# Performance work log

Measured on AMD Instinct MI355X. Metric: run time of the kernel, lower is better.

Reference implementation:

```python
import jax, jax.numpy as jnp
import numpy as np
from jax.scipy.special import logsumexp

HIDDEN = 512
KEY_DIM = HIDDEN // 8  # 64
B, N, M = 4, 2048, 2048
EPS_IN = 1e-5  # InstanceNorm2d default eps
N_ITERS = 20


def setup_inputs() -> dict:
    key = jax.random.key(0)
    k = jax.random.split(key, 6)
    bound = 1.0 / np.sqrt(HIDDEN)  # nn.Linear default init range
    return {
        "x": jax.random.normal(k[0], (B, N, HIDDEN), dtype=jnp.float32),
        "y": jax.random.normal(k[1], (B, M, HIDDEN), dtype=jnp.float32),
        "Wq": jax.random.uniform(k[2], (KEY_DIM, HIDDEN), jnp.float32, -bound, bound),
        "bq": jax.random.uniform(k[3], (KEY_DIM,), jnp.float32, -bound, bound),
        "in_w": jnp.ones((1,), jnp.float32),   # InstanceNorm2d affine weight
        "in_b": jnp.zeros((1,), jnp.float32),  # InstanceNorm2d affine bias
    }


def _sinkhorn_slack(log_alpha, n_iters):
    # log_alpha: [B, J, K]; pad with a zero slack row and column -> [B, J+1, K+1]
    la = jnp.pad(log_alpha, ((0, 0), (0, 1), (0, 1)))

    def step(la, _):
        top = la[:, :-1, :]
        top = top - logsumexp(top, axis=2, keepdims=True)
        la = jnp.concatenate([top, la[:, -1:, :]], axis=1)
        left = la[:, :, :-1]
        left = left - logsumexp(left, axis=1, keepdims=True)
        la = jnp.concatenate([left, la[:, :, -1:]], axis=2)
        return la, None

    la, _ = jax.lax.scan(step, la, None, length=n_iters)
    return la[:, :-1, :-1]


def reference(x, y, Wq, bq, in_w, in_b):
    # linear projection to key_dim
    xw = jnp.einsum('bnh,kh->bnk', x, Wq) + bq  # [B,N,K]
    yw = jnp.einsum('bmh,kh->bmk', y, Wq) + bq  # [B,M,K]
    # pairwise squared euclidean distance [B,N,M]
    dist = (jnp.sum(xw * xw, axis=-1)[:, :, None]
            + jnp.sum(yw * yw, axis=-1)[:, None, :]
            - 2.0 * jnp.einsum('bnk,bmk->bnm', xw, yw))
    e = jnp.exp(-dist)
    # InstanceNorm2d(1, affine=True): normalize each [N,M] map per batch element
    mean = jnp.mean(e, axis=(1, 2), keepdims=True)
    var = jnp.mean((e - mean) ** 2, axis=(1, 2), keepdims=True)
    dist_s = (e - mean) / jnp.sqrt(var + EPS_IN) * in_w[0] + in_b[0]
    # 20-iter slack Sinkhorn in log space
    log_ds = _sinkhorn_slack(dist_s, N_ITERS)
    ds = jnp.exp(log_ds)
    atweight = jnp.max(ds, axis=-1, keepdims=True)  # [B,N,1]
    attention = jnp.einsum('bni,bmi->bnm', atweight, atweight)  # [B,N,N]
    return attention
```

## Files before the change

kernel.cpp:

```cpp
#include <hip/hip_runtime.h>
#include <hip/hip_bf16.h>

constexpr int B = 4, N = 2048, M = 2048, H = 512, ITERS = 20;
constexpr float EPS_IN = 1e-5f;
constexpr float LOG2E = 1.4426950408889634f;
constexpr float LN2 = 0.6931471805599453f;

typedef unsigned short ushort_t;
typedef unsigned int uint_t;
typedef __attribute__((ext_vector_type(8))) short bf16x8;
typedef __attribute__((ext_vector_type(4))) float f32x4;

__device__ __forceinline__ float fexp2(float x) { return __builtin_amdgcn_exp2f(x); }
__device__ __forceinline__ float flog2(float x) { return __builtin_amdgcn_logf(x); }
__device__ __forceinline__ float blo(uint_t v) { return __uint_as_float(v << 16); }
__device__ __forceinline__ float bhi(uint_t v) { return __uint_as_float(v & 0xffff0000u); }
__device__ __forceinline__ uint_t bf16rn(float f) {
  uint_t x = __float_as_uint(f);
  return (x + 0x7fffu + ((x >> 16) & 1u)) >> 16;
}

__global__ __launch_bounds__(256) void wqconv_kernel(
    const float* __restrict__ Wq, ushort_t* __restrict__ wqh) {
  int g = blockIdx.x * 256 + threadIdx.x;
  float4 v = *(const float4*)(Wq + (size_t)g * 4);
  uint2 pk;
  pk.x = bf16rn(v.x) | (bf16rn(v.y) << 16);
  pk.y = bf16rn(v.z) | (bf16rn(v.w) << 16);
  *(uint2*)(wqh + (size_t)g * 4) = pk;
}

__global__ __launch_bounds__(256) void proj_kernel(
    const float* __restrict__ x, const float* __restrict__ y,
    const ushort_t* __restrict__ wqh, const float* __restrict__ bq,
    ushort_t* __restrict__ qwh, float* __restrict__ norms,
    float* __restrict__ stats) {
  int t = threadIdx.x;
  if (blockIdx.x == 0 && t < 32) stats[t] = 0.0f;
  int w = t >> 6, lane = t & 63;
  int fr = lane & 15, fh = (lane >> 4) * 8;
  int rw = blockIdx.x * 64 + w * 16;
  int row = rw + fr;
  const float* src = (row < B * N) ? x + (size_t)row * H
                                   : y + (size_t)(row - B * N) * H;

  f32x4 acc[4];
#pragma unroll
  for (int j = 0; j < 4; j++) acc[j] = (f32x4){0.f, 0.f, 0.f, 0.f};

#pragma unroll
  for (int ks = 0; ks < 16; ks++) {
    float4 a0 = *(const float4*)(src + ks * 32 + fh);
    float4 a1 = *(const float4*)(src + ks * 32 + fh + 4);
    union { uint4 u; bf16x8 h; } ac;
    ac.u.x = bf16rn(a0.x) | (bf16rn(a0.y) << 16);
    ac.u.y = bf16rn(a0.z) | (bf16rn(a0.w) << 16);
    ac.u.z = bf16rn(a1.x) | (bf16rn(a1.y) << 16);
    ac.u.w = bf16rn(a1.z) | (bf16rn(a1.w) << 16);
    bf16x8 aF = ac.h;
#pragma unroll
    for (int j = 0; j < 4; j++) {
      bf16x8 bF = *(const bf16x8*)(wqh + (size_t)(j * 16 + fr) * H + ks * 32 + fh);
      acc[j] = __builtin_amdgcn_mfma_f32_16x16x32_bf16(aF, bF, acc[j], 0, 0, 0);
    }
  }

  float bqv[4];
#pragma unroll
  for (int j = 0; j < 4; j++) bqv[j] = bq[j * 16 + fr];

#pragma unroll
  for (int reg = 0; reg < 4; reg++) {
    int r = rw + ((lane >> 4) << 2) + reg;
    float nr = 0.0f;
#pragma unroll
    for (int j = 0; j < 4; j++) {
      float vv = acc[j][reg] + bqv[j];
      qwh[(size_t)r * 64 + j * 16 + fr] = (ushort_t)bf16rn(vv);
      nr = fmaf(vv, vv, nr);
    }
    nr += __shfl_xor(nr, 1, 64);
    nr += __shfl_xor(nr, 2, 64);
    nr += __shfl_xor(nr, 4, 64);
    nr += __shfl_xor(nr, 8, 64);
    if (fr == 0) norms[r] = nr;
  }
}

__global__ __launch_bounds__(256) void dist_kernel(
    const ushort_t* __restrict__ qwh, const float* __restrict__ norms,
    ushort_t* __restrict__ e, float* __restrict__ stats) {
  __shared__ __align__(16) ushort_t eT[128 * 136];
  __shared__ float xnL[128], ynL[128], scr[12];
  int t = threadIdx.x;
  int b = blockIdx.z;
  int n0 = blockIdx.x * 128, m0 = blockIdx.y * 128;
  int w = t >> 6, lane = t & 63;

  if (t < 128) xnL[t] = norms[b * N + n0 + t];
  else ynL[t - 128] = norms[B * N + b * M + m0 + (t - 128)];

  int wr = (w >> 1) * 64, wc = (w & 1) * 64;
  int fr = lane & 15, fk = (lane >> 4) * 8;

  f32x4 acc[4][4];
#pragma unroll
  for (int i = 0; i < 4; i++)
#pragma unroll
    for (int j = 0; j < 4; j++) acc[i][j] = (f32x4){0.f, 0.f, 0.f, 0.f};

  const ushort_t* xb = qwh + (size_t)(b * N + n0 + wr + fr) * 64 + fk;
  const ushort_t* yb = qwh + (size_t)(B * N + b * M + m0 + wc + fr) * 64 + fk;
#pragma unroll
  for (int kg = 0; kg < 2; kg++) {
    bf16x8 aF[4], bF[4];
#pragma unroll
    for (int i = 0; i < 4; i++) {
      aF[i] = *(const bf16x8*)(xb + (size_t)i * 16 * 64 + kg * 32);
      bF[i] = *(const bf16x8*)(yb + (size_t)i * 16 * 64 + kg * 32);
    }
#pragma unroll
    for (int i = 0; i < 4; i++)
#pragma unroll
      for (int j = 0; j < 4; j++)
        acc[i][j] = __builtin_amdgcn_mfma_f32_16x16x32_bf16(
            aF[i], bF[j], acc[i][j], 0, 0, 0);
  }
  __syncthreads();

  float lsum = 0.0f, lsq = 0.0f, lmax = 0.0f;
#pragma unroll
  for (int i = 0; i < 4; i++) {
    int rl = wr + i * 16 + ((lane >> 4) << 2);
    float xn0 = xnL[rl], xn1 = xnL[rl + 1], xn2 = xnL[rl + 2], xn3 = xnL[rl + 3];
#pragma unroll
    for (int j = 0; j < 4; j++) {
      int cl = wc + j * 16 + (lane & 15);
      float yn_ = ynL[cl];
      float v0 = __expf(-(xn0 + yn_ - 2.0f * acc[i][j][0]));
      float v1 = __expf(-(xn1 + yn_ - 2.0f * acc[i][j][1]));
      float v2 = __expf(-(xn2 + yn_ - 2.0f * acc[i][j][2]));
      float v3 = __expf(-(xn3 + yn_ - 2.0f * acc[i][j][3]));
      lsum += (v0 + v1) + (v2 + v3);
      lsq += (v0 * v0 + v1 * v1) + (v2 * v2 + v3 * v3);
      lmax = fmaxf(fmaxf(lmax, fmaxf(v0, v1)), fmaxf(v2, v3));
      eT[(rl + 0) * 136 + cl] = (ushort_t)bf16rn(v0);
      eT[(rl + 1) * 136 + cl] = (ushort_t)bf16rn(v1);
      eT[(rl + 2) * 136 + cl] = (ushort_t)bf16rn(v2);
      eT[(rl + 3) * 136 + cl] = (ushort_t)bf16rn(v3);
    }
  }
#pragma unroll
  for (int off = 32; off; off >>= 1) {
    lsum += __shfl_xor(lsum, off, 64);
    lsq += __shfl_xor(lsq, off, 64);
    lmax = fmaxf(lmax, __shfl_xor(lmax, off, 64));
  }
  if (lane == 0) { scr[w] = lsum; scr[4 + w] = lsq; scr[8 + w] = lmax; }
  __syncthreads();

#pragma unroll
  for (int p = 0; p < 8; p++) {
    int row = p * 16 + (t >> 4);
    int cs = (t & 15) * 8;
    uint4 vv = *(const uint4*)&eT[row * 136 + cs];
    *(uint4*)(e + (size_t)(b * N + n0 + row) * M + m0 + cs) = vv;
  }
  if (t == 0) {
    float ssum = scr[0] + scr[1] + scr[2] + scr[3];
    float ssq = scr[4] + scr[5] + scr[6] + scr[7];
    float smax = fmaxf(fmaxf(scr[8], scr[9]), fmaxf(scr[10], scr[11]));
    atomicAdd(&stats[b * 4 + 0], ssum);
    atomicAdd(&stats[b * 4 + 1], ssq);
    atomicMax((unsigned int*)&stats[b * 4 + 2], __float_as_uint(smax));
  }
}

__global__ void params_csinit_kernel(const float* __restrict__ stats,
                                     const float* __restrict__ in_w,
                                     const float* __restrict__ in_b,
                                     float* __restrict__ params,
                                     float* __restrict__ csb) {
  int g = blockIdx.x * 256 + threadIdx.x;
  *(float4*)(csb + g * 4) = float4{0.f, 0.f, 0.f, 0.f};
  if (blockIdx.x == 0 && threadIdx.x < B) {
    int b = threadIdx.x;
    float NMf = (float)N * (float)M;
    float mean = stats[b * 4 + 0] / NMf;
    float var = stats[b * 4 + 1] / NMf - mean * mean;
    var = fmaxf(var, 0.0f);
    float stdv = sqrtf(var + EPS_IN);
    float s = in_w[0] / stdv;
    float t = in_b[0] - mean * s;
    float emax = __uint_as_float(((const unsigned int*)stats)[b * 4 + 2]);
    float Amax = fmaxf(fmaf(s, emax, t), t);
    float KK = fmaxf(Amax - 60.0f, 0.0f);
    params[b * 8 + 0] = s * LOG2E;
    params[b * 8 + 1] = (t - 2.0f * KK) * LOG2E;
    params[b * 8 + 2] = KK;
    params[b * 8 + 3] = __expf(-KK);
    params[b * 8 + 4] = __expf(KK);
  }
}

#define PASS1(uu, off, PA, PB)                           \
  {                                                      \
    float4 ca = *(const float4*)&C2a[(off) + ln4];       \
    float4 cb = *(const float4*)&C2b[(off) + ln4];       \
    PA.x = fexp2(fmaf(blo(uu.x), sL, ca.x));             \
    PA.y = fexp2(fmaf(bhi(uu.x), sL, ca.y));             \
    PA.z = fexp2(fmaf(blo(uu.y), sL, ca.z));             \
    PA.w = fexp2(fmaf(bhi(uu.y), sL, ca.w));             \
    PB.x = fexp2(fmaf(blo(uu.z), sL, cb.x));             \
    PB.y = fexp2(fmaf(bhi(uu.z), sL, cb.y));             \
    PB.z = fexp2(fmaf(blo(uu.w), sL, cb.z));             \
    PB.w = fexp2(fmaf(bhi(uu.w), sL, cb.w));             \
    s0 += PA.x + PB.x;                                   \
    s1 += PA.y + PB.y;                                   \
    s2 += PA.z + PB.z;                                   \
    s3 += PA.w + PB.w;                                   \
  }

#define PASS2(PA, PB, AA, BB)                            \
  {                                                      \
    AA.x = fmaf(PA.x, g, AA.x);                          \
    AA.y = fmaf(PA.y, g, AA.y);                          \
    AA.z = fmaf(PA.z, g, AA.z);                          \
    AA.w = fmaf(PA.w, g, AA.w);                          \
    BB.x = fmaf(PB.x, g, BB.x);                          \
    BB.y = fmaf(PB.y, g, BB.y);                          \
    BB.z = fmaf(PB.z, g, BB.z);                          \
    BB.w = fmaf(PB.w, g, BB.w);                          \
  }

#define DO_ROW(q0, q1, q2, q3, ridx)                                   \
  {                                                                    \
    float s0 = 0, s1 = 0, s2 = 0, s3 = 0;                              \
    PASS1(q0, 0, pA0, pB0)                                             \
    PASS1(q1, 256, pA1, pB1)                                           \
    PASS1(q2, 512, pA2, pB2)                                           \
    PASS1(q3, 768, pA3, pB3)                                           \
    float sum = (s0 + s1) + (s2 + s3);                                 \
    _Pragma("unroll")                                                  \
    for (int off = 32; off; off >>= 1) sum += __shfl_xor(sum, off, 64);\
    float sumtot = sum + enk;                                          \
    float ls = flog2(sumtot);                                          \
    if (lane == 0) R[b * N + (ridx)] = KK + LN2 * ls;                  \
    float g = fexp2(-KK * LOG2E - ls);                                 \
    PASS2(pA0, pB0, accA0, accB0)                                      \
    PASS2(pA1, pB1, accA1, accB1)                                      \
    PASS2(pA2, pB2, accA2, accB2)                                      \
    PASS2(pA3, pB3, accA3, accB3)                                      \
  }

__global__ __launch_bounds__(256) void sink_pass(
    const ushort_t* __restrict__ e, const float* __restrict__ params,
    const float* __restrict__ cs_cur, float* __restrict__ cs_nxt,
    float* __restrict__ cs_zz, float* __restrict__ R) {
  __shared__ __align__(16) float C2a[1024], C2b[1024];
  __shared__ __align__(16) float Ds[2048];
  __shared__ __align__(16) float colA[1024], colB[1024];
  int t = threadIdx.x;
  int b = blockIdx.y, blk = blockIdx.x;
  int w = t >> 6, lane = t & 63;
  int ln4 = lane * 4;
  const float* pr = params + b * 8;
  float sL = pr[0], c0L = pr[1], KK = pr[2], enk = pr[3], ekk = pr[4];

  int r0 = blk * 16 + w * 4;
  const ushort_t* ep = e + (size_t)(b * N + r0) * M + lane * 8;
  uint4 u0 = *(const uint4*)(ep);
  uint4 u1 = *(const uint4*)(ep + 512);
  uint4 u2 = *(const uint4*)(ep + 1024);
  uint4 u3 = *(const uint4*)(ep + 1536);
  const ushort_t* ep2 = ep + M;
  uint4 v0 = *(const uint4*)(ep2);
  uint4 v1 = *(const uint4*)(ep2 + 512);
  uint4 v2 = *(const uint4*)(ep2 + 1024);
  uint4 v3 = *(const uint4*)(ep2 + 1536);

  if (blk == 0) {
#pragma unroll
    for (int k = 0; k < 2; k++)
      *(float4*)(cs_zz + b * M + (k * 256 + t) * 4) = float4{0.f, 0.f, 0.f, 0.f};
  }
  {
    float4 c0 = *(const float4*)(cs_cur + b * M + t * 8);
    float4 c1 = *(const float4*)(cs_cur + b * M + t * 8 + 4);
    c0.x += enk; c0.y += enk; c0.z += enk; c0.w += enk;
    c1.x += enk; c1.y += enk; c1.z += enk; c1.w += enk;
    float4 ca, cb;
    ca.x = c0L - flog2(c0.x); ca.y = c0L - flog2(c0.y);
    ca.z = c0L - flog2(c0.z); ca.w = c0L - flog2(c0.w);
    cb.x = c0L - flog2(c1.x); cb.y = c0L - flog2(c1.y);
    cb.z = c0L - flog2(c1.z); cb.w = c0L - flog2(c1.w);
    *(float4*)&C2a[w * 256 + ln4] = ca;
    *(float4*)&C2b[w * 256 + ln4] = cb;
    float4 d0 = {ekk * c0.x, ekk * c0.y, ekk * c0.z, ekk * c0.w};
    float4 d1 = {ekk * c1.x, ekk * c1.y, ekk * c1.z, ekk * c1.w};
    *(float4*)&Ds[t * 8] = d0;
    *(float4*)&Ds[t * 8 + 4] = d1;
  }
  __syncthreads();

  float4 accA0 = {0,0,0,0}, accA1 = {0,0,0,0}, accA2 = {0,0,0,0}, accA3 = {0,0,0,0};
  float4 accB0 = {0,0,0,0}, accB1 = {0,0,0,0}, accB2 = {0,0,0,0}, accB3 = {0,0,0,0};
  float4 pA0, pA1, pA2, pA3, pB0, pB1, pB2, pB3;

  DO_ROW(u0, u1, u2, u3, r0)
  {
    const ushort_t* ep3 = ep + 2 * M;
    u0 = *(const uint4*)(ep3);
    u1 = *(const uint4*)(ep3 + 512);
    u2 = *(const uint4*)(ep3 + 1024);
    u3 = *(const uint4*)(ep3 + 1536);
  }
  DO_ROW(v0, v1, v2, v3, r0 + 1)
  {
    const ushort_t* ep4 = ep + 3 * M;
    v0 = *(const uint4*)(ep4);
    v1 = *(const uint4*)(ep4 + 512);
    v2 = *(const uint4*)(ep4 + 1024);
    v3 = *(const uint4*)(ep4 + 1536);
  }
  DO_ROW(u0, u1, u2, u3, r0 + 2)
  DO_ROW(v0, v1, v2, v3, r0 + 3)

  for (int ww = 0; ww < 4; ww++) {
    if (w == ww) {
      if (ww == 0) {
        *(float4*)&colA[ln4] = accA0;
        *(float4*)&colA[256 + ln4] = accA1;
        *(float4*)&colA[512 + ln4] = accA2;
        *(float4*)&colA[768 + ln4] = accA3;
        *(float4*)&colB[ln4] = accB0;
        *(float4*)&colB[256 + ln4] = accB1;
        *(float4*)&colB[512 + ln4] = accB2;
        *(float4*)&colB[768 + ln4] = accB3;
      } else {
        float4 q;
        q = *(float4*)&colA[ln4];
        q.x += accA0.x; q.y += accA0.y; q.z += accA0.z; q.w += accA0.w;
        *(float4*)&colA[ln4] = q;
        q = *(float4*)&colA[256 + ln4];
        q.x += accA1.x; q.y += accA1.y; q.z += accA1.z; q.w += accA1.w;
        *(float4*)&colA[256 + ln4] = q;
        q = *(float4*)&colA[512 + ln4];
        q.x += accA2.x; q.y += accA2.y; q.z += accA2.z; q.w += accA2.w;
        *(float4*)&colA[512 + ln4] = q;
        q = *(float4*)&colA[768 + ln4];
        q.x += accA3.x; q.y += accA3.y; q.z += accA3.z; q.w += accA3.w;
        *(float4*)&colA[768 + ln4] = q;
        q = *(float4*)&colB[ln4];
        q.x += accB0.x; q.y += accB0.y; q.z += accB0.z; q.w += accB0.w;
        *(float4*)&colB[ln4] = q;
        q = *(float4*)&colB[256 + ln4];
        q.x += accB1.x; q.y += accB1.y; q.z += accB1.z; q.w += accB1.w;
        *(float4*)&colB[256 + ln4] = q;
        q = *(float4*)&colB[512 + ln4];
        q.x += accB2.x; q.y += accB2.y; q.z += accB2.z; q.w += accB2.w;
        *(float4*)&colB[512 + ln4] = q;
        q = *(float4*)&colB[768 + ln4];
        q.x += accB3.x; q.y += accB3.y; q.z += accB3.z; q.w += accB3.w;
        *(float4*)&colB[768 + ln4] = q;
      }
    }
    __syncthreads();
  }
  {
    int q = t & 7;
    const float* srcb = (q < 4) ? colA : colB;
    int qq = q & 3;
#pragma unroll
    for (int k = 0; k < 8; k++) {
      int j = k * 256 + t;
      int idx = (j >> 9) * 256 + ((j >> 3) & 63) * 4 + qq;
      atomicAdd(&cs_nxt[b * M + j], srcb[idx] * Ds[j]);
    }
  }
}

__global__ __launch_bounds__(256) void awmax_kernel(
    const ushort_t* __restrict__ e, const float* __restrict__ params,
    const float* __restrict__ cs_fin, const float* __restrict__ R,
    float* __restrict__ aw) {
  __shared__ __align__(16) float C2a[1024], C2b[1024];
  int t = threadIdx.x;
  int b = blockIdx.y, blk = blockIdx.x;
  const float* pr = params + b * 8;
  float sL = pr[0], c0L = pr[1], KK = pr[2], enk = pr[3];
  {
    float4 v0 = *(const float4*)(cs_fin + b * M + t * 8);
    float4 v1 = *(const float4*)(cs_fin + b * M + t * 8 + 4);
    float4 ca, cb;
    ca.x = c0L - flog2(v0.x + enk); ca.y = c0L - flog2(v0.y + enk);
    ca.z = c0L - flog2(v0.z + enk); ca.w = c0L - flog2(v0.w + enk);
    cb.x = c0L - flog2(v1.x + enk); cb.y = c0L - flog2(v1.y + enk);
    cb.z = c0L - flog2(v1.z + enk); cb.w = c0L - flog2(v1.w + enk);
    int it = t >> 6, ln = t & 63;
    *(float4*)&C2a[it * 256 + ln * 4] = ca;
    *(float4*)&C2b[it * 256 + ln * 4] = cb;
  }
  __syncthreads();

  int w = t >> 6, lane = t & 63;
  int ln4 = lane * 4;
  int r0 = blk * 16 + w * 4;
  const ushort_t* erow = e + (size_t)(b * N + r0) * M;
#pragma unroll
  for (int rr = 0; rr < 4; rr++) {
    float mx = -3.4e38f;
#pragma unroll
    for (int it = 0; it < 4; it++) {
      uint4 u = *(const uint4*)(erow + (size_t)rr * M + it * 512 + lane * 8);
      float4 ca = *(const float4*)&C2a[it * 256 + ln4];
      float4 cb = *(const float4*)&C2b[it * 256 + ln4];
      mx = fmaxf(mx, fmaf(blo(u.x), sL, ca.x));
      mx = fmaxf(mx, fmaf(bhi(u.x), sL, ca.y));
      mx = fmaxf(mx, fmaf(blo(u.y), sL, ca.z));
      mx = fmaxf(mx, fmaf(bhi(u.y), sL, ca.w));
      mx = fmaxf(mx, fmaf(blo(u.z), sL, cb.x));
      mx = fmaxf(mx, fmaf(bhi(u.z), sL, cb.y));
      mx = fmaxf(mx, fmaf(blo(u.w), sL, cb.z));
      mx = fmaxf(mx, fmaf(bhi(u.w), sL, cb.w));
    }
#pragma unroll
    for (int off = 32; off; off >>= 1) mx = fmaxf(mx, __shfl_xor(mx, off, 64));
    if (lane == 0) {
      float Rr = R[b * N + r0 + rr];
      aw[b * N + r0 + rr] = fexp2(mx + (KK - Rr) * LOG2E);
    }
  }
}

__global__ __launch_bounds__(256) void outer_kernel(const float* __restrict__ aw,
                                                    float* __restrict__ out) {
  size_t idx = (size_t)blockIdx.x * 256 + threadIdx.x;
  int b = (int)(idx >> 20);
  size_t rem = idx & ((1u << 20) - 1);
  int n = (int)(rem >> 9);
  int m4 = (int)(rem & 511) << 2;
  float a = aw[b * N + n];
  float4 wv = *(const float4*)(aw + b * N + m4);
  float4 o = {a * wv.x, a * wv.y, a * wv.z, a * wv.w};
  *(float4*)(out + (idx << 2)) = o;
}

extern "C" void kernel_launch(void* const* d_in, const int* in_sizes, int n_in,
                              void* d_out, int out_size, void* d_ws, size_t ws_size,
                              hipStream_t stream) {
  const float* x = (const float*)d_in[0];
  const float* y = (const float*)d_in[1];
  const float* Wq = (const float*)d_in[2];
  const float* bq = (const float*)d_in[3];
  const float* in_w = (const float*)d_in[4];
  const float* in_b = (const float*)d_in[5];
  ushort_t* e = (ushort_t*)d_out;

  float* ws = (float*)d_ws;
  ushort_t* qwh = (ushort_t*)ws;
  float* norms = ws + 1048576;
  float* R = norms + 16384;
  float* csb0 = R + 8192;
  float* csb1 = csb0 + 8192;
  float* csb2 = csb1 + 8192;
  float* aw = csb2 + 8192;
  float* stats = aw + 8192;
  float* params = stats + 32;
  ushort_t* wqh = (ushort_t*)(params + 32);
  float* csb[3] = {csb0, csb1, csb2};

  wqconv_kernel<<<32, 256, 0, stream>>>(Wq, wqh);
  proj_kernel<<<256, 256, 0, stream>>>(x, y, wqh, bq, qwh, norms, stats);
  dist_kernel<<<dim3(16, 16, B), 256, 0, stream>>>(qwh, norms, e, stats);
  params_csinit_kernel<<<24, 256, 0, stream>>>(stats, in_w, in_b, params, csb0);

  for (int it = 0; it < ITERS; it++) {
    sink_pass<<<dim3(128, B), 256, 0, stream>>>(
        e, params, csb[it % 3], csb[(it + 1) % 3], csb[(it + 2) % 3], R);
  }
  awmax_kernel<<<dim3(128, B), 256, 0, stream>>>(e, params, csb[ITERS % 3], R, aw);
  outer_kernel<<<16384, 256, 0, stream>>>(aw, (float*)d_out);
}
```

Measured before the change: 307.3 us.

## Double sinkhorn block size to 512 threads and pre-swizzle projection layout for MFMA

The Sinkhorn pass now uses 512-thread blocks that each cover 32 rows, with half as many blocks. Column partials go into two shared-memory accumulators that are summed before the atomic adds, which halves the number of global atomics per column. Separately, the projection output is written in a fragment-contiguous layout so the distance kernel's MFMA operand loads become fully coalesced per lane. The cost is fewer blocks in the Sinkhorn pass (256 total), which may lower parallelism, plus more shared memory per block.

```diff
diff --git a/kernel.cpp b/kernel.cpp
--- a/kernel.cpp
+++ b/kernel.cpp
@@ -33,7 +33,7 @@
 __global__ __launch_bounds__(256) void proj_kernel(
     const float* __restrict__ x, const float* __restrict__ y,
     const ushort_t* __restrict__ wqh, const float* __restrict__ bq,
-    ushort_t* __restrict__ qwh, float* __restrict__ norms,
+    ushort_t* __restrict__ qwf, float* __restrict__ norms,
     float* __restrict__ stats) {
   int t = threadIdx.x;
   if (blockIdx.x == 0 && t < 32) stats[t] = 0.0f;
@@ -69,14 +69,17 @@
 #pragma unroll
   for (int j = 0; j < 4; j++) bqv[j] = bq[j * 16 + fr];
 
+  size_t gbase = (size_t)(rw >> 4) * 1024;
 #pragma unroll
   for (int reg = 0; reg < 4; reg++) {
-    int r = rw + ((lane >> 4) << 2) + reg;
+    int rr = ((lane >> 4) << 2) + reg;
+    int r = rw + rr;
     float nr = 0.0f;
 #pragma unroll
     for (int j = 0; j < 4; j++) {
       float vv = acc[j][reg] + bqv[j];
-      qwh[(size_t)r * 64 + j * 16 + fr] = (ushort_t)bf16rn(vv);
+      qwf[gbase + (size_t)(j * 2 + (fr >> 3)) * 128 + rr * 8 + (fr & 7)] =
+          (ushort_t)bf16rn(vv);
       nr = fmaf(vv, vv, nr);
     }
     nr += __shfl_xor(nr, 1, 64);
@@ -88,7 +91,7 @@
 }
 
 __global__ __launch_bounds__(256) void dist_kernel(
-    const ushort_t* __restrict__ qwh, const float* __restrict__ norms,
+    const ushort_t* __restrict__ qwf, const float* __restrict__ norms,
     ushort_t* __restrict__ e, float* __restrict__ stats) {
   __shared__ __align__(16) ushort_t eT[128 * 136];
   __shared__ float xnL[128], ynL[128], scr[12];
@@ -101,7 +104,6 @@
   else ynL[t - 128] = norms[B * N + b * M + m0 + (t - 128)];
 
   int wr = (w >> 1) * 64, wc = (w & 1) * 64;
-  int fr = lane & 15, fk = (lane >> 4) * 8;
 
   f32x4 acc[4][4];
 #pragma unroll
@@ -109,15 +111,15 @@
 #pragma unroll
     for (int j = 0; j < 4; j++) acc[i][j] = (f32x4){0.f, 0.f, 0.f, 0.f};
 
-  const ushort_t* xb = qwh + (size_t)(b * N + n0 + wr + fr) * 64 + fk;
-  const ushort_t* yb = qwh + (size_t)(B * N + b * M + m0 + wc + fr) * 64 + fk;
+  const ushort_t* xg = qwf + (size_t)((b * N + n0 + wr) >> 4) * 1024 + lane * 8;
+  const ushort_t* yg = qwf + (size_t)((B * N + b * M + m0 + wc) >> 4) * 1024 + lane * 8;
 #pragma unroll
   for (int kg = 0; kg < 2; kg++) {
     bf16x8 aF[4], bF[4];
 #pragma unroll
     for (int i = 0; i < 4; i++) {
-      aF[i] = *(const bf16x8*)(xb + (size_t)i * 16 * 64 + kg * 32);
-      bF[i] = *(const bf16x8*)(yb + (size_t)i * 16 * 64 + kg * 32);
+      aF[i] = *(const bf16x8*)(xg + (size_t)i * 1024 + kg * 512);
+      bF[i] = *(const bf16x8*)(yg + (size_t)i * 1024 + kg * 512);
     }
 #pragma unroll
     for (int i = 0; i < 4; i++)
@@ -253,13 +255,55 @@
     PASS2(pA3, pB3, accA3, accB3)                                      \
   }
 
-__global__ __launch_bounds__(256) void sink_pass(
+#define COMBINE8(cA, cB)                                               \
+  {                                                                    \
+    float4 q;                                                          \
+    q = *(float4*)&cA[ln4];                                            \
+    q.x += accA0.x; q.y += accA0.y; q.z += accA0.z; q.w += accA0.w;    \
+    *(float4*)&cA[ln4] = q;                                            \
+    q = *(float4*)&cA[256 + ln4];                                      \
+    q.x += accA1.x; q.y += accA1.y; q.z += accA1.z; q.w += accA1.w;    \
+    *(float4*)&cA[256 + ln4] = q;                                      \
+    q = *(float4*)&cA[512 + ln4];                                      \
+    q.x += accA2.x; q.y += accA2.y; q.z += accA2.z; q.w += accA2.w;    \
+    *(float4*)&cA[512 + ln4] = q;                                      \
+    q = *(float4*)&cA[768 + ln4];                                      \
+    q.x += accA3.x; q.y += accA3.y; q.z += accA3.z; q.w += accA3.w;    \
+    *(float4*)&cA[768 + ln4] = q;                                      \
+    q = *(float4*)&cB[ln4];                                            \
+    q.x += accB0.x; q.y += accB0.y; q.z += accB0.z; q.w += accB0.w;    \
+    *(float4*)&cB[ln4] = q;                                            \
+    q = *(float4*)&cB[256 + ln4];                                      \
+    q.x += accB1.x; q.y += accB1.y; q.z += accB1.z; q.w += accB1.w;    \
+    *(float4*)&cB[256 + ln4] = q;                                      \
+    q = *(float4*)&cB[512 + ln4];                                      \
+    q.x += accB2.x; q.y += accB2.y; q.z += accB2.z; q.w += accB2.w;    \
+    *(float4*)&cB[512 + ln4] = q;                                      \
+    q = *(float4*)&cB[768 + ln4];                                      \
+    q.x += accB3.x; q.y += accB3.y; q.z += accB3.z; q.w += accB3.w;    \
+    *(float4*)&cB[768 + ln4] = q;                                      \
+  }
+
+#define STORE8(cA, cB)                                                 \
+  {                                                                    \
+    *(float4*)&cA[ln4] = accA0;                                        \
+    *(float4*)&cA[256 + ln4] = accA1;                                  \
+    *(float4*)&cA[512 + ln4] = accA2;                                  \
+    *(float4*)&cA[768 + ln4] = accA3;                                  \
+    *(float4*)&cB[ln4] = accB0;                                        \
+    *(float4*)&cB[256 + ln4] = accB1;                                  \
+    *(float4*)&cB[512 + ln4] = accB2;                                  \
+    *(float4*)&cB[768 + ln4] = accB3;                                  \
+  }
+
+__global__ __launch_bounds__(512) void sink_pass(
     const ushort_t* __restrict__ e, const float* __restrict__ params,
     const float* __restrict__ cs_cur, float* __restrict__ cs_nxt,
     float* __restrict__ cs_zz, float* __restrict__ R) {
   __shared__ __align__(16) float C2a[1024], C2b[1024];
   __shared__ __align__(16) float Ds[2048];
   __shared__ __align__(16) float colA[1024], colB[1024];
+  __shared__ __align__(16) float colA2[1024], colB2[1024];
   int t = threadIdx.x;
   int b = blockIdx.y, blk = blockIdx.x;
   int w = t >> 6, lane = t & 63;
@@ -267,7 +311,7 @@
   const float* pr = params + b * 8;
   float sL = pr[0], c0L = pr[1], KK = pr[2], enk = pr[3], ekk = pr[4];
 
-  int r0 = blk * 16 + w * 4;
+  int r0 = blk * 32 + w * 4;
   const ushort_t* ep = e + (size_t)(b * N + r0) * M + lane * 8;
   uint4 u0 = *(const uint4*)(ep);
   uint4 u1 = *(const uint4*)(ep + 512);
@@ -280,11 +324,9 @@
   uint4 v3 = *(const uint4*)(ep2 + 1536);
 
   if (blk == 0) {
-#pragma unroll
-    for (int k = 0; k < 2; k++)
-      *(float4*)(cs_zz + b * M + (k * 256 + t) * 4) = float4{0.f, 0.f, 0.f, 0.f};
-  }
-  {
+    *(float4*)(cs_zz + b * M + t * 4) = float4{0.f, 0.f, 0.f, 0.f};
+  }
+  if (t < 256) {
     float4 c0 = *(const float4*)(cs_cur + b * M + t * 8);
     float4 c1 = *(const float4*)(cs_cur + b * M + t * 8 + 4);
     c0.x += enk; c0.y += enk; c0.z += enk; c0.w += enk;
@@ -328,54 +370,22 @@
 
   for (int ww = 0; ww < 4; ww++) {
     if (w == ww) {
-      if (ww == 0) {
-        *(float4*)&colA[ln4] = accA0;
-        *(float4*)&colA[256 + ln4] = accA1;
-        *(float4*)&colA[512 + ln4] = accA2;
-        *(float4*)&colA[768 + ln4] = accA3;
-        *(float4*)&colB[ln4] = accB0;
-        *(float4*)&colB[256 + ln4] = accB1;
-        *(float4*)&colB[512 + ln4] = accB2;
-        *(float4*)&colB[768 + ln4] = accB3;
-      } else {
-        float4 q;
-        q = *(float4*)&colA[ln4];
-        q.x += accA0.x; q.y += accA0.y; q.z += accA0.z; q.w += accA0.w;
-        *(float4*)&colA[ln4] = q;
-        q = *(float4*)&colA[256 + ln4];
-        q.x += accA1.x; q.y += accA1.y; q.z += accA1.z; q.w += accA1.w;
-        *(float4*)&colA[256 + ln4] = q;
-        q = *(float4*)&colA[512 + ln4];
-        q.x += accA2.x; q.y += accA2.y; q.z += accA2.z; q.w += accA2.w;
-        *(float4*)&colA[512 + ln4] = q;
-        q = *(float4*)&colA[768 + ln4];
-        q.x += accA3.x; q.y += accA3.y; q.z += accA3.z; q.w += accA3.w;
-        *(float4*)&colA[768 + ln4] = q;
-        q = *(float4*)&colB[ln4];
-        q.x += accB0.x; q.y += accB0.y; q.z += accB0.z; q.w += accB0.w;
-        *(float4*)&colB[ln4] = q;
-        q = *(float4*)&colB[256 + ln4];
-        q.x += accB1.x; q.y += accB1.y; q.z += accB1.z; q.w += accB1.w;
-        *(float4*)&colB[256 + ln4] = q;
-        q = *(float4*)&colB[512 + ln4];
-        q.x += accB2.x; q.y += accB2.y; q.z += accB2.z; q.w += accB2.w;
-        *(float4*)&colB[512 + ln4] = q;
-        q = *(float4*)&colB[768 + ln4];
-        q.x += accB3.x; q.y += accB3.y; q.z += accB3.z; q.w += accB3.w;
-        *(float4*)&colB[768 + ln4] = q;
-      }
+      if (ww == 0) STORE8(colA, colB) else COMBINE8(colA, colB)
+    } else if (w == ww + 4) {
+      if (ww == 0) STORE8(colA2, colB2) else COMBINE8(colA2, colB2)
     }
     __syncthreads();
   }
   {
     int q = t & 7;
-    const float* srcb = (q < 4) ? colA : colB;
+    const float* s1 = (q < 4) ? colA : colB;
+    const float* s2 = (q < 4) ? colA2 : colB2;
     int qq = q & 3;
 #pragma unroll
-    for (int k = 0; k < 8; k++) {
-      int j = k * 256 + t;
+    for (int k = 0; k < 4; k++) {
+      int j = k * 512 + t;
       int idx = (j >> 9) * 256 + ((j >> 3) & 63) * 4 + qq;
-      atomicAdd(&cs_nxt[b * M + j], srcb[idx] * Ds[j]);
+      atomicAdd(&cs_nxt[b * M + j], (s1[idx] + s2[idx]) * Ds[j]);
     }
   }
 }
@@ -458,7 +468,7 @@
   ushort_t* e = (ushort_t*)d_out;
 
   float* ws = (float*)d_ws;
-  ushort_t* qwh = (ushort_t*)ws;
+  ushort_t* qwf = (ushort_t*)ws;
   float* norms = ws + 1048576;
   float* R = norms + 16384;
   float* csb0 = R + 8192;
@@ -471,12 +481,12 @@
   float* csb[3] = {csb0, csb1, csb2};
 
   wqconv_kernel<<<32, 256, 0, stream>>>(Wq, wqh);
-  proj_kernel<<<256, 256, 0, stream>>>(x, y, wqh, bq, qwh, norms, stats);
-  dist_kernel<<<dim3(16, 16, B), 256, 0, stream>>>(qwh, norms, e, stats);
+  proj_kernel<<<256, 256, 0, stream>>>(x, y, wqh, bq, qwf, norms, stats);
+  dist_kernel<<<dim3(16, 16, B), 256, 0, stream>>>(qwf, norms, e, stats);
   params_csinit_kernel<<<24, 256, 0, stream>>>(stats, in_w, in_b, params, csb0);
 
   for (int it = 0; it < ITERS; it++) {
-    sink_pass<<<dim3(128, B), 256, 0, stream>>>(
+    sink_pass<<<dim3(64, B), 512, 0, stream>>>(
         e, params, csb[it % 3], csb[(it + 1) % 3], csb[(it + 2) % 3], R);
   }
   awmax_kernel<<<dim3(128, B), 256, 0, stream>>>(e, params, csb[ITERS % 3], R, aw);
```

Result: faster. 266.1 us (-13.4%).
